# Kernel tuning notes

Measured on AMD Instinct MI355X. Metric: run time of the kernel, lower is better.

Reference implementation:

```python
import jax, jax.numpy as jnp
import numpy as np

HEADS = 16
DIM_HEAD = 64
ROT_DIM = 32  # RotaryEmbedding(dim=dim_head//2) -> rotates first 32 channels
SCALE = DIM_HEAD ** -0.5


def _rope(x):
    # x: [b, h, n, d]; rotate first ROT_DIM channels, interleaved pairs (lucidrains style)
    n = x.shape[2]
    inv_freq = 1.0 / (10000.0 ** (jnp.arange(0, ROT_DIM, 2, dtype=jnp.float32) / ROT_DIM))  # [16]
    ang = jnp.arange(n, dtype=jnp.float32)[:, None] * inv_freq[None, :]  # [n, 16]
    cos, sin = jnp.cos(ang), jnp.sin(ang)  # [n, 16]
    x_rot, x_pass = x[..., :ROT_DIM], x[..., ROT_DIM:]
    x1 = x_rot[..., 0::2]  # [b,h,n,16]
    x2 = x_rot[..., 1::2]
    y1 = x1 * cos - x2 * sin
    y2 = x2 * cos + x1 * sin
    y = jnp.stack([y1, y2], axis=-1).reshape(x_rot.shape)  # re-interleave
    return jnp.concatenate([y, x_pass], axis=-1)


def setup_inputs() -> dict:
    key = jax.random.key(0)
    ks = jax.random.split(key, 5)
    b, n, d = 4, 2048, 1024
    inner = HEADS * DIM_HEAD
    return {
        "queries": jax.random.normal(ks[0], (b, n, d), jnp.float32),
        "Wq": jax.random.normal(ks[1], (d, inner), jnp.float32) * (d ** -0.5),
        "Wkv": jax.random.normal(ks[2], (d, 2 * inner), jnp.float32) * (d ** -0.5),
        "Wout": jax.random.normal(ks[3], (inner, d), jnp.float32) * (inner ** -0.5),
        "bout": jnp.zeros((d,), jnp.float32),
    }


def reference(queries, Wq, Wkv, Wout, bout):
    b, n, _ = queries.shape
    q = queries @ Wq                      # [b,n,inner]
    kv = queries @ Wkv                    # self-attention: context = queries
    k, v = jnp.split(kv, 2, axis=-1)
    split_heads = lambda t: t.reshape(b, n, HEADS, DIM_HEAD).transpose(0, 2, 1, 3)
    q, k, v = split_heads(q), split_heads(k), split_heads(v)
    q, k = _rope(q), _rope(k)
    sim = jnp.einsum('bhid,bhjd->bhij', q, k) * SCALE
    attn = jax.nn.softmax(sim, axis=-1)
    out = jnp.einsum('bhij,bhjd->bhid', attn, v)
    out = out.transpose(0, 2, 1, 3).reshape(b, n, HEADS * DIM_HEAD)
    return out @ Wout + bout
```

## Files before the change

### kernel.cpp

```cpp
#include <hip/hip_runtime.h>
#include <math.h>

#define BB    4
#define NN    2048
#define DD    1024
#define HH    16
#define DHD   64
#define INNER 1024
#define LOG2_10K_D16 0.8304820237218406f
#define SCALE_LOG2E 0.1803368801111601f

typedef short bf16x8 __attribute__((ext_vector_type(8)));
typedef short bf16x4 __attribute__((ext_vector_type(4)));
typedef float f32x4  __attribute__((ext_vector_type(4)));
typedef unsigned short u16x8 __attribute__((ext_vector_type(8)));

#define ASYNC16(g, l) __builtin_amdgcn_global_load_lds( \
    (const __attribute__((address_space(1))) void*)(g),  \
    (__attribute__((address_space(3))) void*)(l), 16, 0, 0)

#define MFMA16(a, b, c) __builtin_amdgcn_mfma_f32_16x16x32_bf16((a), (b), (c), 0, 0, 0)

static __device__ __forceinline__ float fexp2(float x) {
#if __has_builtin(__builtin_amdgcn_exp2f)
    return __builtin_amdgcn_exp2f(x);
#else
    float r;
    asm("v_exp_f32 %0, %1" : "=v"(r) : "v"(x));
    return r;
#endif
}

static __device__ __forceinline__ unsigned short f2bf(float f) {
    union { float f; unsigned int u; } v; v.f = f;
    unsigned int u = v.u;
    u += 0x7fffu + ((u >> 16) & 1u);
    return (unsigned short)(u >> 16);
}
static __device__ __forceinline__ unsigned int packbf2(float lo, float hi) {
    union { float f; unsigned int u; } a, b;
    a.f = lo; b.f = hi;
    return __builtin_amdgcn_perm(b.u + 0x8000u, a.u + 0x8000u, 0x07060302u);
}

__global__ __launch_bounds__(256) void cast_x_kernel(
    const float* __restrict__ X, unsigned short* __restrict__ Xb)
{
    const size_t i = ((size_t)blockIdx.x * 256 + threadIdx.x) * 8;
    const float4 a = *(const float4*)(X + i);
    const float4 b = *(const float4*)(X + i + 4);
    u16x8 o;
    o[0] = f2bf(a.x); o[1] = f2bf(a.y); o[2] = f2bf(a.z); o[3] = f2bf(a.w);
    o[4] = f2bf(b.x); o[5] = f2bf(b.y); o[6] = f2bf(b.z); o[7] = f2bf(b.w);
    *(u16x8*)(Xb + i) = o;
}

__global__ __launch_bounds__(256) void tcast_kernel(
    const float* __restrict__ src, unsigned short* __restrict__ dst,
    int K, int N)
{
    __shared__ float ts[32][33];
    const int t = threadIdx.x;
    const int n0 = blockIdx.x * 32, k0 = blockIdx.y * 32;
    const int r = t >> 5, c = t & 31;
    #pragma unroll
    for (int p = 0; p < 4; ++p)
        ts[r + p * 8][c] = src[(size_t)(k0 + r + p * 8) * N + n0 + c];
    __syncthreads();
    #pragma unroll
    for (int p = 0; p < 4; ++p)
        dst[(size_t)(n0 + r + p * 8) * K + k0 + c] = f2bf(ts[c][r + p * 8]);
}

__global__ __launch_bounds__(256) void proj_qkv_mfma(
    const unsigned short* __restrict__ Xb, const unsigned short* __restrict__ Wt,
    unsigned short* __restrict__ qb, unsigned short* __restrict__ kb,
    unsigned short* __restrict__ vb)
{
    __shared__ __align__(16) unsigned short As[128 * 32];
    __shared__ __align__(16) unsigned short Bs[128 * 32];

    const int t     = threadIdx.x;
    const int w     = t >> 6, lane = t & 63;
    const int lane4 = lane & 15, quad = lane >> 4, quad8 = quad * 8;
    const int wm    = w >> 1, wn = w & 1;
    const int m0    = blockIdx.y * 128, n0 = blockIdx.x * 128;

    const int srow = t >> 2, scol = (t & 3) * 8;
    const unsigned short* gA = Xb + (size_t)(m0 + srow) * DD + scol;
    const unsigned short* gB = Wt + (size_t)(n0 + srow) * DD + scol;
    unsigned short* lA = As + t * 8;
    unsigned short* lB = Bs + t * 8;

    f32x4 acc[4][4] = {};

    for (int k0 = 0; k0 < DD; k0 += 32) {
        __syncthreads();
        ASYNC16(gA + k0,            lA);
        ASYNC16(gA + 64 * DD + k0,  lA + 2048);
        ASYNC16(gB + k0,            lB);
        ASYNC16(gB + 64 * DD + k0,  lB + 2048);
        __syncthreads();

        bf16x8 a[4], b[4];
        #pragma unroll
        for (int i = 0; i < 4; ++i)
            a[i] = *(const bf16x8*)&As[(wm * 64 + i * 16 + lane4) * 32 + quad8];
        #pragma unroll
        for (int j = 0; j < 4; ++j)
            b[j] = *(const bf16x8*)&Bs[(wn * 64 + j * 16 + lane4) * 32 + quad8];
        #pragma unroll
        for (int i = 0; i < 4; ++i)
            #pragma unroll
            for (int j = 0; j < 4; ++j)
                acc[i][j] = MFMA16(a[i], b[j], acc[i][j]);
    }

    const int sec = n0 >> 10;

    if (sec == 2) {
        #pragma unroll
        for (int j = 0; j < 4; ++j) {
            const int csec = (n0 & 1023) + wn * 64 + j * 16;
            const int h    = csec >> 6;
            const int dh   = (csec & 63) + lane4;
            #pragma unroll
            for (int i = 0; i < 4; ++i) {
                const int rg0 = m0 + wm * 64 + i * 16 + quad * 4;
                const int b   = rg0 >> 11;
                const int n   = rg0 & 2047;
                uint2 pk;
                pk.x = packbf2(acc[i][j][0], acc[i][j][1]);
                pk.y = packbf2(acc[i][j][2], acc[i][j][3]);
                *(uint2*)(vb + (((size_t)b * HH + h) * DHD + dh) * NN + n) = pk;
            }
        }
    } else {
        unsigned short* dst = (sec == 0) ? qb : kb;
        const float qscale = (sec == 0) ? SCALE_LOG2E : 1.0f;
        #pragma unroll
        for (int j = 0; j < 4; ++j) {
            const int csec = (n0 & 1023) + wn * 64 + j * 16;
            const int h    = csec >> 6;
            const int dhb  = csec & 63;
            const int dh   = dhb + lane4;
            const bool rope = (dhb < 32);
            const float invf = fexp2(-(float)(dh >> 1) * LOG2_10K_D16);
            #pragma unroll
            for (int i = 0; i < 4; ++i) {
                #pragma unroll
                for (int r = 0; r < 4; ++r) {
                    const int rg = m0 + wm * 64 + i * 16 + quad * 4 + r;
                    const int b  = rg >> 11;
                    const int n  = rg & 2047;
                    float x = acc[i][j][r] * qscale;
                    if (rope) {
                        const float ang = (float)n * invf;
                        float s_, c_;
                        __sincosf(ang, &s_, &c_);
                        const float p = __shfl_xor(x, 1);
                        x = (lane4 & 1) ? fmaf(p, s_, x * c_)
                                        : fmaf(p, -s_, x * c_);
                    }
                    dst[(((size_t)b * HH + h) * NN + n) * DHD + dh] = f2bf(x);
                }
            }
        }
    }
}

__global__ __launch_bounds__(256, 2) void attn_kernel(
    const unsigned short* __restrict__ qb, const unsigned short* __restrict__ kb,
    const unsigned short* __restrict__ vtb, unsigned short* __restrict__ aob)
{
    __shared__ __align__(16) unsigned char smem[65536];
    unsigned short (*ks)[128][64] = (unsigned short (*)[128][64])smem;
    unsigned short (*vs)[64][128] = (unsigned short (*)[64][128])(smem + 32768);

    const int t     = threadIdx.x;
    const int kq    = t >> 6;
    const int lane  = t & 63;
    const int lane4 = lane & 15;
    const int quad  = lane >> 4;
    const int quad8 = quad * 8;
    const int l7    = lane4 & 7;

    const int bid = blockIdx.x;
    const int bh  = bid & 63;
    const int q0  = (bid >> 6) * 64;
    const size_t hb = (size_t)bh * NN * DHD;

    bf16x8 qf[4][2];
    #pragma unroll
    for (int qt = 0; qt < 4; ++qt) {
        const unsigned short* qrow = qb + hb + (size_t)(q0 + qt * 16 + lane4) * DHD;
        qf[qt][0] = *(const bf16x8*)(qrow + quad8);
        qf[qt][1] = *(const bf16x8*)(qrow + 32 + quad8);
    }

    bf16x8 onesf;
    #pragma unroll
    for (int j = 0; j < 8; ++j) onesf[j] = (short)0x3F80;

    const int krow  = kq * 16 + (lane >> 3);
    const int kslot = ((lane & 7) ^ (lane >> 3)) * 8;
    const unsigned short* kg = kb + hb + (size_t)krow * DHD + (lane & 7) * 8;

    const int vrow0 = lane >> 2;
    const int vm    = 2 * kq + (lane & 1) + ((lane >> 1) & 1) * 8;
    const int vr7   = vrow0 & 7;
    const int halfo = (vm >> 3) * 4;
    const int colA  = ((((vm & 7) * 2)     ^ vr7) * 8) + halfo;
    const int colB  = ((((vm & 7) * 2 + 1) ^ vr7) * 8) + halfo;
    const unsigned short* vg = vtb + hb + (size_t)vrow0 * NN + vm * 8;

    f32x4 o[4][4], lacc[4];
    #pragma unroll
    for (int d = 0; d < 4; ++d)
        #pragma unroll
        for (int qt = 0; qt < 4; ++qt) o[d][qt] = (f32x4){0.f, 0.f, 0.f, 0.f};
    #pragma unroll
    for (int qt = 0; qt < 4; ++qt) lacc[qt] = (f32x4){0.f, 0.f, 0.f, 0.f};

    {
        const bf16x8 k0 = *(const bf16x8*)(kg);
        const bf16x8 k1 = *(const bf16x8*)(kg + 8 * DHD);
        const bf16x8 k2 = *(const bf16x8*)(kg + 64 * DHD);
        const bf16x8 k3 = *(const bf16x8*)(kg + 72 * DHD);
        const bf16x8 v0 = *(const bf16x8*)(vg);
        const bf16x8 v1 = *(const bf16x8*)(vg + (size_t)16 * NN);
        const bf16x8 v2 = *(const bf16x8*)(vg + (size_t)32 * NN);
        const bf16x8 v3 = *(const bf16x8*)(vg + (size_t)48 * NN);
        *(bf16x8*)&ks[0][krow][kslot]      = k0;
        *(bf16x8*)&ks[0][krow + 8][kslot]  = k1;
        *(bf16x8*)&ks[0][krow + 64][kslot] = k2;
        *(bf16x8*)&ks[0][krow + 72][kslot] = k3;
        #pragma unroll
        for (int s = 0; s < 4; ++s) {
            const bf16x8 vv = (s == 0) ? v0 : (s == 1) ? v1 : (s == 2) ? v2 : v3;
            bf16x4 lo = __builtin_shufflevector(vv, vv, 0, 1, 2, 3);
            bf16x4 hi = __builtin_shufflevector(vv, vv, 4, 5, 6, 7);
            *(bf16x4*)&vs[0][vrow0 + 16 * s][colA] = lo;
            *(bf16x4*)&vs[0][vrow0 + 16 * s][colB] = hi;
        }
    }

    for (int kt = 0; kt < NN / 128; ++kt) {
        const int cur = kt & 1;
        const bool more = (kt + 1 < NN / 128);

        bf16x8 nk0, nk1, nk2, nk3, nv0, nv1, nv2, nv3;
        if (more) {
            const unsigned short* kgn = kg + (size_t)(kt + 1) * 128 * DHD;
            const unsigned short* vgn = vg + (kt + 1) * 128;
            nk0 = *(const bf16x8*)(kgn);
            nk1 = *(const bf16x8*)(kgn + 8 * DHD);
            nk2 = *(const bf16x8*)(kgn + 64 * DHD);
            nk3 = *(const bf16x8*)(kgn + 72 * DHD);
            nv0 = *(const bf16x8*)(vgn);
            nv1 = *(const bf16x8*)(vgn + (size_t)16 * NN);
            nv2 = *(const bf16x8*)(vgn + (size_t)32 * NN);
            nv3 = *(const bf16x8*)(vgn + (size_t)48 * NN);
        }

        bf16x8 ak[2][2];
        #pragma unroll
        for (int sub = 0; sub < 2; ++sub) {
            const int row = sub * 64 + kq * 16 + lane4;
            ak[sub][0] = *(const bf16x8*)&ks[cur][row][(quad ^ l7) * 8];
            ak[sub][1] = *(const bf16x8*)&ks[cur][row][((quad + 4) ^ l7) * 8];
        }

        bf16x8 pb[4];
        #pragma unroll
        for (int qt = 0; qt < 4; ++qt) {
            f32x4 z0 = (f32x4){0.f, 0.f, 0.f, 0.f};
            f32x4 z1 = (f32x4){0.f, 0.f, 0.f, 0.f};
            z0 = MFMA16(ak[0][0], qf[qt][0], z0);
            z0 = MFMA16(ak[0][1], qf[qt][1], z0);
            z1 = MFMA16(ak[1][0], qf[qt][0], z1);
            z1 = MFMA16(ak[1][1], qf[qt][1], z1);
            union { unsigned int u[4]; bf16x8 v; } pk;
            pk.u[0] = packbf2(fexp2(z0[0]), fexp2(z0[1]));
            pk.u[1] = packbf2(fexp2(z0[2]), fexp2(z0[3]));
            pk.u[2] = packbf2(fexp2(z1[0]), fexp2(z1[1]));
            pk.u[3] = packbf2(fexp2(z1[2]), fexp2(z1[3]));
            pb[qt] = pk.v;
            lacc[qt] = MFMA16(onesf, pb[qt], lacc[qt]);
        }

        #pragma unroll
        for (int d = 0; d < 4; ++d) {
            const bf16x8 av = *(const bf16x8*)&vs[cur][d * 16 + lane4][((kq * 4 + quad) ^ l7) * 8];
            #pragma unroll
            for (int qt = 0; qt < 4; ++qt)
                o[d][qt] = MFMA16(av, pb[qt], o[d][qt]);
        }

        if (more) {
            const int nb = cur ^ 1;
            *(bf16x8*)&ks[nb][krow][kslot]      = nk0;
            *(bf16x8*)&ks[nb][krow + 8][kslot]  = nk1;
            *(bf16x8*)&ks[nb][krow + 64][kslot] = nk2;
            *(bf16x8*)&ks[nb][krow + 72][kslot] = nk3;
            #pragma unroll
            for (int s = 0; s < 4; ++s) {
                const bf16x8 vv = (s == 0) ? nv0 : (s == 1) ? nv1 : (s == 2) ? nv2 : nv3;
                bf16x4 lo = __builtin_shufflevector(vv, vv, 0, 1, 2, 3);
                bf16x4 hi = __builtin_shufflevector(vv, vv, 4, 5, 6, 7);
                *(bf16x4*)&vs[nb][vrow0 + 16 * s][colA] = lo;
                *(bf16x4*)&vs[nb][vrow0 + 16 * s][colB] = hi;
            }
        }
    }

    __syncthreads();
    float* pbuf = (float*)smem;
    #pragma unroll
    for (int d = 0; d < 4; ++d)
        #pragma unroll
        for (int qt = 0; qt < 4; ++qt)
            #pragma unroll
            for (int r = 0; r < 4; ++r)
                pbuf[(kq * 64 + d * 16 + quad * 4 + r) * 64 + qt * 16 + lane4] = o[d][qt][r];
    __syncthreads();

    f32x4 of[4];
    #pragma unroll
    for (int d = 0; d < 4; ++d)
        #pragma unroll
        for (int r = 0; r < 4; ++r) {
            const int dh = d * 16 + quad * 4 + r;
            const int qc = kq * 16 + lane4;
            of[d][r] = pbuf[dh * 64 + qc] + pbuf[(64 + dh) * 64 + qc]
                     + pbuf[(128 + dh) * 64 + qc] + pbuf[(192 + dh) * 64 + qc];
        }
    __syncthreads();

    if (quad == 0) {
        #pragma unroll
        for (int qt = 0; qt < 4; ++qt)
            pbuf[(kq * 4 + qt) * 16 + lane4] = lacc[qt][0];
    }
    __syncthreads();
    const float lt = pbuf[(0 * 4 + kq) * 16 + lane4] + pbuf[(1 * 4 + kq) * 16 + lane4]
                   + pbuf[(2 * 4 + kq) * 16 + lane4] + pbuf[(3 * 4 + kq) * 16 + lane4];
    const float linv = 1.0f / lt;

    const int b = bh >> 4, h = bh & 15;
    const int n = q0 + kq * 16 + lane4;
    unsigned short* obase = aob + ((size_t)b * NN + n) * INNER + h * DHD;
    #pragma unroll
    for (int d = 0; d < 4; ++d) {
        uint2 pk;
        pk.x = packbf2(of[d][0] * linv, of[d][1] * linv);
        pk.y = packbf2(of[d][2] * linv, of[d][3] * linv);
        *(uint2*)(obase + d * 16 + quad * 4) = pk;
    }
}

__global__ __launch_bounds__(256) void out_proj_mfma(
    const unsigned short* __restrict__ Ab, const unsigned short* __restrict__ Wt,
    const float* __restrict__ bias, float* __restrict__ C)
{
    __shared__ __align__(16) unsigned short As[128 * 32];
    __shared__ __align__(16) unsigned short Bs[128 * 32];

    const int t     = threadIdx.x;
    const int w     = t >> 6, lane = t & 63;
    const int lane4 = lane & 15, quad = lane >> 4, quad8 = quad * 8;
    const int wm    = w >> 1, wn = w & 1;
    const int m0    = blockIdx.y * 128, n0 = blockIdx.x * 128;

    const int srow = t >> 2, scol = (t & 3) * 8;
    const unsigned short* gA = Ab + (size_t)(m0 + srow) * INNER + scol;
    const unsigned short* gB = Wt + (size_t)(n0 + srow) * INNER + scol;
    unsigned short* lA = As + t * 8;
    unsigned short* lB = Bs + t * 8;

    f32x4 acc[4][4] = {};

    for (int k0 = 0; k0 < INNER; k0 += 32) {
        __syncthreads();
        ASYNC16(gA + k0,               lA);
        ASYNC16(gA + 64 * INNER + k0,  lA + 2048);
        ASYNC16(gB + k0,               lB);
        ASYNC16(gB + 64 * INNER + k0,  lB + 2048);
        __syncthreads();

        bf16x8 a[4], b[4];
        #pragma unroll
        for (int i = 0; i < 4; ++i)
            a[i] = *(const bf16x8*)&As[(wm * 64 + i * 16 + lane4) * 32 + quad8];
        #pragma unroll
        for (int j = 0; j < 4; ++j)
            b[j] = *(const bf16x8*)&Bs[(wn * 64 + j * 16 + lane4) * 32 + quad8];
        #pragma unroll
        for (int i = 0; i < 4; ++i)
            #pragma unroll
            for (int j = 0; j < 4; ++j)
                acc[i][j] = MFMA16(a[i], b[j], acc[i][j]);
    }

    #pragma unroll
    for (int j = 0; j < 4; ++j) {
        const int col = n0 + wn * 64 + j * 16 + lane4;
        const float bv = bias[col];
        #pragma unroll
        for (int i = 0; i < 4; ++i)
            #pragma unroll
            for (int r = 0; r < 4; ++r) {
                const int rg = m0 + wm * 64 + i * 16 + quad * 4 + r;
                C[(size_t)rg * DD + col] = acc[i][j][r] + bv;
            }
    }
}

extern "C" void kernel_launch(void* const* d_in, const int* in_sizes, int n_in,
                              void* d_out, int out_size, void* d_ws, size_t ws_size,
                              hipStream_t stream)
{
    const float* X    = (const float*)d_in[0];
    const float* Wq   = (const float*)d_in[1];
    const float* Wkv  = (const float*)d_in[2];
    const float* Wout = (const float*)d_in[3];
    const float* bout = (const float*)d_in[4];
    float* out = (float*)d_out;

    const size_t E = (size_t)BB * HH * NN * DHD;
    unsigned short* qb  = (unsigned short*)d_ws;
    unsigned short* kb  = qb + E;
    unsigned short* vtb = kb + E;
    unsigned short* xb  = vtb + E;
    unsigned short* wt  = xb + E;
    unsigned short* wo  = wt + (size_t)3072 * 1024;

    cast_x_kernel<<<4096, 256, 0, stream>>>(X, xb);
    tcast_kernel<<<dim3(32, 32), 256, 0, stream>>>(Wq,   wt,               1024, 1024);
    tcast_kernel<<<dim3(64, 32), 256, 0, stream>>>(Wkv,  wt + 1024 * 1024, 1024, 2048);
    tcast_kernel<<<dim3(32, 32), 256, 0, stream>>>(Wout, wo,               1024, 1024);

    proj_qkv_mfma<<<dim3(3072 / 128, 8192 / 128), 256, 0, stream>>>(
        xb, wt, qb, kb, vtb);

    attn_kernel<<<dim3(NN / 64 * BB * HH), 256, 0, stream>>>(qb, kb, vtb, xb);

    out_proj_mfma<<<dim3(1024 / 128, 8192 / 128), 256, 0, stream>>>(
        xb, wo, bout, out);
}
```

Baseline: 312.2 us.

## Single-buffer K/V LDS tiles and halve epilogue scratch to raise occupancy

Drops the K/V double buffer in shared memory, which halves LDS use to 32KB. The launch bound rises from 2 to 5 so more blocks can sit on each CU. The epilogue reduction is also restructured: two warps store partial outputs and the other two add into them, with XOR-swizzled columns, so the scratch fits in the smaller LDS. The intent is more overlap from occupancy in place of explicit double buffering. The tighter launch bound risks register spills, and the single buffer relies on each wave touching only its own rows.

After: 880.8 us. 182% more time.

```diff
diff --git a/kernel.cpp b/kernel.cpp
--- a/kernel.cpp
+++ b/kernel.cpp
@@ -169,13 +169,13 @@
     }
 }
 
-__global__ __launch_bounds__(256, 2) void attn_kernel(
+__global__ __launch_bounds__(256, 5) void attn_kernel(
     const unsigned short* __restrict__ qb, const unsigned short* __restrict__ kb,
     const unsigned short* __restrict__ vtb, unsigned short* __restrict__ aob)
 {
-    __shared__ __align__(16) unsigned char smem[65536];
-    unsigned short (*ks)[128][64] = (unsigned short (*)[128][64])smem;
-    unsigned short (*vs)[64][128] = (unsigned short (*)[64][128])(smem + 32768);
+    __shared__ __align__(16) unsigned char smem[32768];
+    unsigned short (*ks)[64]  = (unsigned short (*)[64])smem;
+    unsigned short (*vs)[128] = (unsigned short (*)[128])(smem + 16384);
 
     const int t     = threadIdx.x;
     const int kq    = t >> 6;
@@ -231,22 +231,21 @@
         const bf16x8 v1 = *(const bf16x8*)(vg + (size_t)16 * NN);
         const bf16x8 v2 = *(const bf16x8*)(vg + (size_t)32 * NN);
         const bf16x8 v3 = *(const bf16x8*)(vg + (size_t)48 * NN);
-        *(bf16x8*)&ks[0][krow][kslot]      = k0;
-        *(bf16x8*)&ks[0][krow + 8][kslot]  = k1;
-        *(bf16x8*)&ks[0][krow + 64][kslot] = k2;
-        *(bf16x8*)&ks[0][krow + 72][kslot] = k3;
+        *(bf16x8*)&ks[krow][kslot]      = k0;
+        *(bf16x8*)&ks[krow + 8][kslot]  = k1;
+        *(bf16x8*)&ks[krow + 64][kslot] = k2;
+        *(bf16x8*)&ks[krow + 72][kslot] = k3;
         #pragma unroll
         for (int s = 0; s < 4; ++s) {
             const bf16x8 vv = (s == 0) ? v0 : (s == 1) ? v1 : (s == 2) ? v2 : v3;
             bf16x4 lo = __builtin_shufflevector(vv, vv, 0, 1, 2, 3);
             bf16x4 hi = __builtin_shufflevector(vv, vv, 4, 5, 6, 7);
-            *(bf16x4*)&vs[0][vrow0 + 16 * s][colA] = lo;
-            *(bf16x4*)&vs[0][vrow0 + 16 * s][colB] = hi;
+            *(bf16x4*)&vs[vrow0 + 16 * s][colA] = lo;
+            *(bf16x4*)&vs[vrow0 + 16 * s][colB] = hi;
         }
     }
 
     for (int kt = 0; kt < NN / 128; ++kt) {
-        const int cur = kt & 1;
         const bool more = (kt + 1 < NN / 128);
 
         bf16x8 nk0, nk1, nk2, nk3, nv0, nv1, nv2, nv3;
@@ -267,8 +266,8 @@
         #pragma unroll
         for (int sub = 0; sub < 2; ++sub) {
             const int row = sub * 64 + kq * 16 + lane4;
-            ak[sub][0] = *(const bf16x8*)&ks[cur][row][(quad ^ l7) * 8];
-            ak[sub][1] = *(const bf16x8*)&ks[cur][row][((quad + 4) ^ l7) * 8];
+            ak[sub][0] = *(const bf16x8*)&ks[row][(quad ^ l7) * 8];
+            ak[sub][1] = *(const bf16x8*)&ks[row][((quad + 4) ^ l7) * 8];
         }
 
         bf16x8 pb[4];
@@ -291,50 +290,72 @@
 
         #pragma unroll
         for (int d = 0; d < 4; ++d) {
-            const bf16x8 av = *(const bf16x8*)&vs[cur][d * 16 + lane4][((kq * 4 + quad) ^ l7) * 8];
+            const bf16x8 av = *(const bf16x8*)&vs[d * 16 + lane4][((kq * 4 + quad) ^ l7) * 8];
             #pragma unroll
             for (int qt = 0; qt < 4; ++qt)
                 o[d][qt] = MFMA16(av, pb[qt], o[d][qt]);
         }
 
         if (more) {
-            const int nb = cur ^ 1;
-            *(bf16x8*)&ks[nb][krow][kslot]      = nk0;
-            *(bf16x8*)&ks[nb][krow + 8][kslot]  = nk1;
-            *(bf16x8*)&ks[nb][krow + 64][kslot] = nk2;
-            *(bf16x8*)&ks[nb][krow + 72][kslot] = nk3;
+            *(bf16x8*)&ks[krow][kslot]      = nk0;
+            *(bf16x8*)&ks[krow + 8][kslot]  = nk1;
+            *(bf16x8*)&ks[krow + 64][kslot] = nk2;
+            *(bf16x8*)&ks[krow + 72][kslot] = nk3;
             #pragma unroll
             for (int s = 0; s < 4; ++s) {
                 const bf16x8 vv = (s == 0) ? nv0 : (s == 1) ? nv1 : (s == 2) ? nv2 : nv3;
                 bf16x4 lo = __builtin_shufflevector(vv, vv, 0, 1, 2, 3);
                 bf16x4 hi = __builtin_shufflevector(vv, vv, 4, 5, 6, 7);
-                *(bf16x4*)&vs[nb][vrow0 + 16 * s][colA] = lo;
-                *(bf16x4*)&vs[nb][vrow0 + 16 * s][colB] = hi;
+                *(bf16x4*)&vs[vrow0 + 16 * s][colA] = lo;
+                *(bf16x4*)&vs[vrow0 + 16 * s][colB] = hi;
             }
         }
     }
 
     __syncthreads();
     float* pbuf = (float*)smem;
-    #pragma unroll
-    for (int d = 0; d < 4; ++d)
-        #pragma unroll
-        for (int qt = 0; qt < 4; ++qt)
-            #pragma unroll
-            for (int r = 0; r < 4; ++r)
-                pbuf[(kq * 64 + d * 16 + quad * 4 + r) * 64 + qt * 16 + lane4] = o[d][qt][r];
+
+    if (kq < 2) {
+        #pragma unroll
+        for (int d = 0; d < 4; ++d)
+            #pragma unroll
+            for (int qt = 0; qt < 4; ++qt) {
+                const int col = (qt * 16 + lane4) ^ (quad << 4);
+                #pragma unroll
+                for (int r = 0; r < 4; ++r) {
+                    const int dh = d * 16 + quad * 4 + r;
+                    pbuf[(kq * 64 + dh) * 64 + col] = o[d][qt][r];
+                }
+            }
+    }
+    __syncthreads();
+    if (kq >= 2) {
+        #pragma unroll
+        for (int d = 0; d < 4; ++d)
+            #pragma unroll
+            for (int qt = 0; qt < 4; ++qt) {
+                const int col = (qt * 16 + lane4) ^ (quad << 4);
+                #pragma unroll
+                for (int r = 0; r < 4; ++r) {
+                    const int dh = d * 16 + quad * 4 + r;
+                    const int idx = ((kq - 2) * 64 + dh) * 64 + col;
+                    pbuf[idx] += o[d][qt][r];
+                }
+            }
+    }
     __syncthreads();
 
     f32x4 of[4];
-    #pragma unroll
-    for (int d = 0; d < 4; ++d)
-        #pragma unroll
-        for (int r = 0; r < 4; ++r) {
-            const int dh = d * 16 + quad * 4 + r;
-            const int qc = kq * 16 + lane4;
-            of[d][r] = pbuf[dh * 64 + qc] + pbuf[(64 + dh) * 64 + qc]
-                     + pbuf[(128 + dh) * 64 + qc] + pbuf[(192 + dh) * 64 + qc];
-        }
+    {
+        const int qcol = (kq * 16 + lane4) ^ (quad << 4);
+        #pragma unroll
+        for (int d = 0; d < 4; ++d)
+            #pragma unroll
+            for (int r = 0; r < 4; ++r) {
+                const int dh = d * 16 + quad * 4 + r;
+                of[d][r] = pbuf[dh * 64 + qcol] + pbuf[(64 + dh) * 64 + qcol];
+            }
+    }
     __syncthreads();
 
     if (quad == 0) {
```

## Software-pipeline attention loop: compute next tile's QK scores while doing PV

Applied to the files above, without the earlier changes.

Restructures the attention inner loop so the QK^T MFMAs and exp2 for tile kt+1 are issued alongside the PV MFMAs of tile kt. Global prefetch now runs two tiles ahead. The prologue loads two K/V tiles and computes the first probability tile. The aim is to hide the exp/transcendental latency and MFMA dependency chains, at the cost of more live registers (scn, pb), which may hurt occupancy or cause spills. The reuse of buffer cur for the kt+2 write relies on synchronization that is not visible here.

New measurement: 301.7 us. -3.4%, faster.

```diff
diff --git a/kernel.cpp b/kernel.cpp
--- a/kernel.cpp
+++ b/kernel.cpp
@@ -223,55 +223,60 @@
     for (int qt = 0; qt < 4; ++qt) lacc[qt] = (f32x4){0.f, 0.f, 0.f, 0.f};
 
     {
-        const bf16x8 k0 = *(const bf16x8*)(kg);
-        const bf16x8 k1 = *(const bf16x8*)(kg + 8 * DHD);
-        const bf16x8 k2 = *(const bf16x8*)(kg + 64 * DHD);
-        const bf16x8 k3 = *(const bf16x8*)(kg + 72 * DHD);
-        const bf16x8 v0 = *(const bf16x8*)(vg);
-        const bf16x8 v1 = *(const bf16x8*)(vg + (size_t)16 * NN);
-        const bf16x8 v2 = *(const bf16x8*)(vg + (size_t)32 * NN);
-        const bf16x8 v3 = *(const bf16x8*)(vg + (size_t)48 * NN);
-        *(bf16x8*)&ks[0][krow][kslot]      = k0;
-        *(bf16x8*)&ks[0][krow + 8][kslot]  = k1;
-        *(bf16x8*)&ks[0][krow + 64][kslot] = k2;
-        *(bf16x8*)&ks[0][krow + 72][kslot] = k3;
+        const bf16x8 a0 = *(const bf16x8*)(kg);
+        const bf16x8 a1 = *(const bf16x8*)(kg + 8 * DHD);
+        const bf16x8 a2 = *(const bf16x8*)(kg + 64 * DHD);
+        const bf16x8 a3 = *(const bf16x8*)(kg + 72 * DHD);
+        const bf16x8 b0 = *(const bf16x8*)(vg);
+        const bf16x8 b1 = *(const bf16x8*)(vg + (size_t)16 * NN);
+        const bf16x8 b2 = *(const bf16x8*)(vg + (size_t)32 * NN);
+        const bf16x8 b3 = *(const bf16x8*)(vg + (size_t)48 * NN);
+        const unsigned short* kg1 = kg + (size_t)128 * DHD;
+        const unsigned short* vg1 = vg + 128;
+        const bf16x8 c0 = *(const bf16x8*)(kg1);
+        const bf16x8 c1 = *(const bf16x8*)(kg1 + 8 * DHD);
+        const bf16x8 c2 = *(const bf16x8*)(kg1 + 64 * DHD);
+        const bf16x8 c3 = *(const bf16x8*)(kg1 + 72 * DHD);
+        const bf16x8 d0 = *(const bf16x8*)(vg1);
+        const bf16x8 d1 = *(const bf16x8*)(vg1 + (size_t)16 * NN);
+        const bf16x8 d2 = *(const bf16x8*)(vg1 + (size_t)32 * NN);
+        const bf16x8 d3 = *(const bf16x8*)(vg1 + (size_t)48 * NN);
+
+        *(bf16x8*)&ks[0][krow][kslot]      = a0;
+        *(bf16x8*)&ks[0][krow + 8][kslot]  = a1;
+        *(bf16x8*)&ks[0][krow + 64][kslot] = a2;
+        *(bf16x8*)&ks[0][krow + 72][kslot] = a3;
         #pragma unroll
         for (int s = 0; s < 4; ++s) {
-            const bf16x8 vv = (s == 0) ? v0 : (s == 1) ? v1 : (s == 2) ? v2 : v3;
+            const bf16x8 vv = (s == 0) ? b0 : (s == 1) ? b1 : (s == 2) ? b2 : b3;
             bf16x4 lo = __builtin_shufflevector(vv, vv, 0, 1, 2, 3);
             bf16x4 hi = __builtin_shufflevector(vv, vv, 4, 5, 6, 7);
             *(bf16x4*)&vs[0][vrow0 + 16 * s][colA] = lo;
             *(bf16x4*)&vs[0][vrow0 + 16 * s][colB] = hi;
         }
-    }
-
-    for (int kt = 0; kt < NN / 128; ++kt) {
-        const int cur = kt & 1;
-        const bool more = (kt + 1 < NN / 128);
-
-        bf16x8 nk0, nk1, nk2, nk3, nv0, nv1, nv2, nv3;
-        if (more) {
-            const unsigned short* kgn = kg + (size_t)(kt + 1) * 128 * DHD;
-            const unsigned short* vgn = vg + (kt + 1) * 128;
-            nk0 = *(const bf16x8*)(kgn);
-            nk1 = *(const bf16x8*)(kgn + 8 * DHD);
-            nk2 = *(const bf16x8*)(kgn + 64 * DHD);
-            nk3 = *(const bf16x8*)(kgn + 72 * DHD);
-            nv0 = *(const bf16x8*)(vgn);
-            nv1 = *(const bf16x8*)(vgn + (size_t)16 * NN);
-            nv2 = *(const bf16x8*)(vgn + (size_t)32 * NN);
-            nv3 = *(const bf16x8*)(vgn + (size_t)48 * NN);
-        }
-
+        *(bf16x8*)&ks[1][krow][kslot]      = c0;
+        *(bf16x8*)&ks[1][krow + 8][kslot]  = c1;
+        *(bf16x8*)&ks[1][krow + 64][kslot] = c2;
+        *(bf16x8*)&ks[1][krow + 72][kslot] = c3;
+        #pragma unroll
+        for (int s = 0; s < 4; ++s) {
+            const bf16x8 vv = (s == 0) ? d0 : (s == 1) ? d1 : (s == 2) ? d2 : d3;
+            bf16x4 lo = __builtin_shufflevector(vv, vv, 0, 1, 2, 3);
+            bf16x4 hi = __builtin_shufflevector(vv, vv, 4, 5, 6, 7);
+            *(bf16x4*)&vs[1][vrow0 + 16 * s][colA] = lo;
+            *(bf16x4*)&vs[1][vrow0 + 16 * s][colB] = hi;
+        }
+    }
+
+    bf16x8 pb[4];
+    {
         bf16x8 ak[2][2];
         #pragma unroll
         for (int sub = 0; sub < 2; ++sub) {
             const int row = sub * 64 + kq * 16 + lane4;
-            ak[sub][0] = *(const bf16x8*)&ks[cur][row][(quad ^ l7) * 8];
-            ak[sub][1] = *(const bf16x8*)&ks[cur][row][((quad + 4) ^ l7) * 8];
-        }
-
-        bf16x8 pb[4];
+            ak[sub][0] = *(const bf16x8*)&ks[0][row][(quad ^ l7) * 8];
+            ak[sub][1] = *(const bf16x8*)&ks[0][row][((quad + 4) ^ l7) * 8];
+        }
         #pragma unroll
         for (int qt = 0; qt < 4; ++qt) {
             f32x4 z0 = (f32x4){0.f, 0.f, 0.f, 0.f};
@@ -286,7 +291,48 @@
             pk.u[2] = packbf2(fexp2(z1[0]), fexp2(z1[1]));
             pk.u[3] = packbf2(fexp2(z1[2]), fexp2(z1[3]));
             pb[qt] = pk.v;
-            lacc[qt] = MFMA16(onesf, pb[qt], lacc[qt]);
+        }
+    }
+
+    for (int kt = 0; kt < NN / 128; ++kt) {
+        const int cur = kt & 1;
+        const bool more1 = (kt + 1 < NN / 128);
+        const bool more2 = (kt + 2 < NN / 128);
+
+        bf16x8 nk0, nk1, nk2, nk3, nv0, nv1, nv2, nv3;
+        if (more2) {
+            const unsigned short* kgn = kg + (size_t)(kt + 2) * 128 * DHD;
+            const unsigned short* vgn = vg + (kt + 2) * 128;
+            nk0 = *(const bf16x8*)(kgn);
+            nk1 = *(const bf16x8*)(kgn + 8 * DHD);
+            nk2 = *(const bf16x8*)(kgn + 64 * DHD);
+            nk3 = *(const bf16x8*)(kgn + 72 * DHD);
+            nv0 = *(const bf16x8*)(vgn);
+            nv1 = *(const bf16x8*)(vgn + (size_t)16 * NN);
+            nv2 = *(const bf16x8*)(vgn + (size_t)32 * NN);
+            nv3 = *(const bf16x8*)(vgn + (size_t)48 * NN);
+        }
+
+        f32x4 scn[4][2];
+        if (more1) {
+            bf16x8 ak[2][2];
+            #pragma unroll
+            for (int sub = 0; sub < 2; ++sub) {
+                const int row = sub * 64 + kq * 16 + lane4;
+                ak[sub][0] = *(const bf16x8*)&ks[cur ^ 1][row][(quad ^ l7) * 8];
+                ak[sub][1] = *(const bf16x8*)&ks[cur ^ 1][row][((quad + 4) ^ l7) * 8];
+            }
+            #pragma unroll
+            for (int qt = 0; qt < 4; ++qt) {
+                f32x4 z0 = (f32x4){0.f, 0.f, 0.f, 0.f};
+                f32x4 z1 = (f32x4){0.f, 0.f, 0.f, 0.f};
+                z0 = MFMA16(ak[0][0], qf[qt][0], z0);
+                z0 = MFMA16(ak[0][1], qf[qt][1], z0);
+                z1 = MFMA16(ak[1][0], qf[qt][0], z1);
+                z1 = MFMA16(ak[1][1], qf[qt][1], z1);
+                scn[qt][0] = z0;
+                scn[qt][1] = z1;
+            }
         }
 
         #pragma unroll
@@ -296,20 +342,34 @@
             for (int qt = 0; qt < 4; ++qt)
                 o[d][qt] = MFMA16(av, pb[qt], o[d][qt]);
         }
-
-        if (more) {
-            const int nb = cur ^ 1;
-            *(bf16x8*)&ks[nb][krow][kslot]      = nk0;
-            *(bf16x8*)&ks[nb][krow + 8][kslot]  = nk1;
-            *(bf16x8*)&ks[nb][krow + 64][kslot] = nk2;
-            *(bf16x8*)&ks[nb][krow + 72][kslot] = nk3;
+        #pragma unroll
+        for (int qt = 0; qt < 4; ++qt)
+            lacc[qt] = MFMA16(onesf, pb[qt], lacc[qt]);
+
+        if (more1) {
+            #pragma unroll
+            for (int qt = 0; qt < 4; ++qt) {
+                union { unsigned int u[4]; bf16x8 v; } pk;
+                pk.u[0] = packbf2(fexp2(scn[qt][0][0]), fexp2(scn[qt][0][1]));
+                pk.u[1] = packbf2(fexp2(scn[qt][0][2]), fexp2(scn[qt][0][3]));
+                pk.u[2] = packbf2(fexp2(scn[qt][1][0]), fexp2(scn[qt][1][1]));
+                pk.u[3] = packbf2(fexp2(scn[qt][1][2]), fexp2(scn[qt][1][3]));
+                pb[qt] = pk.v;
+            }
+        }
+
+        if (more2) {
+            *(bf16x8*)&ks[cur][krow][kslot]      = nk0;
+            *(bf16x8*)&ks[cur][krow + 8][kslot]  = nk1;
+            *(bf16x8*)&ks[cur][krow + 64][kslot] = nk2;
+            *(bf16x8*)&ks[cur][krow + 72][kslot] = nk3;
             #pragma unroll
             for (int s = 0; s < 4; ++s) {
                 const bf16x8 vv = (s == 0) ? nv0 : (s == 1) ? nv1 : (s == 2) ? nv2 : nv3;
                 bf16x4 lo = __builtin_shufflevector(vv, vv, 0, 1, 2, 3);
                 bf16x4 hi = __builtin_shufflevector(vv, vv, 4, 5, 6, 7);
-                *(bf16x4*)&vs[nb][vrow0 + 16 * s][colA] = lo;
-                *(bf16x4*)&vs[nb][vrow0 + 16 * s][colB] = hi;
+                *(bf16x4*)&vs[cur][vrow0 + 16 * s][colA] = lo;
+                *(bf16x4*)&vs[cur][vrow0 + 16 * s][colB] = hi;
             }
         }
     }
```
